# Performance work log

Hardware: AMD Instinct MI355X
Metric: run time of the kernel (lower is better)

Reference implementation:

```python
import jax, jax.numpy as jnp
import numpy as np

N = 100000      # nodes
E = 1600000     # edges (before self-loops)
IN = 128        # in_feats
EF = 64         # edge_feat_size
H = 4           # num_heads
D = 32          # out_feats per head
NEG_SLOPE = 0.2 # DGL GATConv default leaky_relu slope


def setup_inputs() -> dict:
    key = jax.random.key(0)
    ks = jax.random.split(key, 9)
    return {
        "node_feats": jax.random.normal(ks[0], (N, IN), jnp.float32),
        "edge_feats": jax.random.normal(ks[1], (E, EF), jnp.float32),
        "src": jax.random.randint(ks[2], (E,), 0, N),
        "dst": jax.random.randint(ks[3], (E,), 0, N),
        "W_edge": jax.random.normal(ks[4], (EF, IN), jnp.float32) * 0.05,
        "b_edge": jnp.zeros((IN,), jnp.float32),
        "W_fc": jax.random.normal(ks[5], (IN, H * D), jnp.float32) * 0.05,
        "attn_l": jax.random.normal(ks[6], (H, D), jnp.float32) * 0.05,
        "attn_r": jax.random.normal(ks[7], (H, D), jnp.float32) * 0.05,
        "bias": jnp.zeros((H * D,), jnp.float32),
    }


def reference(node_feats, edge_feats, src, dst, W_edge, b_edge, W_fc, attn_l, attn_r, bias):
    # edge_proj: computed in the original forward but NOT consumed by GATConv
    edge_emb = edge_feats @ W_edge + b_edge  # [E, IN] (dead in original module)
    del edge_emb

    # fc projection, split into heads
    feat = (node_feats @ W_fc).reshape(N, H, D)          # [N, H, D]
    el = jnp.einsum('nhd,hd->nh', feat, attn_l)          # [N, H]
    er = jnp.einsum('nhd,hd->nh', feat, attn_r)          # [N, H]

    # add self-loops (dgl.add_self_loop appends (i, i) for every node)
    loops = jnp.arange(N, dtype=src.dtype)
    s = jnp.concatenate([src, loops])                    # [E + N]
    d = jnp.concatenate([dst, loops])                    # [E + N]

    # per-edge attention logits
    e = jax.nn.leaky_relu(el[s] + er[d], NEG_SLOPE)      # [E+N, H]

    # segment softmax over incoming edges of each destination
    emax = jax.ops.segment_max(e, d, num_segments=N)     # [N, H]
    ee = jnp.exp(e - emax[d])                            # [E+N, H]
    denom = jax.ops.segment_sum(ee, d, num_segments=N)   # [N, H]
    alpha = ee / denom[d]                                # [E+N, H]

    # weighted aggregation of source features per destination
    msg = alpha[:, :, None] * feat[s]                    # [E+N, H, D]
    out = jax.ops.segment_sum(msg, d, num_segments=N)    # [N, H, D]
    out = out + bias.reshape(H, D)
    return out
```

## Files before the change

### kernel.cpp

```cpp
#include <hip/hip_runtime.h>
#include <hip/hip_bf16.h>

#define NEG_SLOPE 0.2f

__device__ __forceinline__ int block_scan_incl(int v, int t, int nwaves, int* wsum) {
    const int lane = t & 63, wid = t >> 6;
#pragma unroll
    for (int off = 1; off < 64; off <<= 1) {
        int u = __shfl_up(v, off);
        if (lane >= off) v += u;
    }
    if (lane == 63) wsum[wid] = v;
    __syncthreads();
    if (wid == 0) {
        int w = (lane < nwaves) ? wsum[lane] : 0;
#pragma unroll
        for (int off = 1; off < 64; off <<= 1) {
            int u = __shfl_up(w, off);
            if (lane >= off) w += u;
        }
        if (lane < nwaves) wsum[lane] = w;
    }
    __syncthreads();
    if (wid > 0) v += wsum[wid - 1];
    return v;
}

__global__ __launch_bounds__(256) void gemm_hist_kernel(
    const float* __restrict__ node, const float* __restrict__ Wfc,
    const float* __restrict__ attn_l, const float* __restrict__ attn_r,
    const int* __restrict__ dst, int* __restrict__ counts,
    __hip_bfloat162* __restrict__ featp,
    float* __restrict__ el, float* __restrict__ er,
    int N_, int E_, int T_)
{
    __shared__ float Xl[32][132];
    __shared__ float Wl[32][132];

    const int t  = threadIdx.x;

    for (int e = blockIdx.x * 256 + t; e < T_; e += gridDim.x * 256) {
        int d = (e < E_) ? dst[e] : (e - E_);
        atomicAdd(&counts[d], 1);
    }

    const int tx = t & 15;
    const int ty = t >> 4;
    const int gr0 = blockIdx.x * 128;

    float acc[8][8];
#pragma unroll
    for (int a = 0; a < 8; a++)
#pragma unroll
        for (int b = 0; b < 8; b++) acc[a][b] = 0.f;

    for (int k0 = 0; k0 < 128; k0 += 32) {
#pragma unroll
        for (int j = 0; j < 16; j++) {
            int i = t + 256 * j;
            int kk = i & 31, row = i >> 5;
            int gr = gr0 + row;
            Xl[kk][row] = (gr < N_) ? node[(size_t)gr * 128 + k0 + kk] : 0.f;
        }
#pragma unroll
        for (int j = 0; j < 16; j++) {
            int i = t + 256 * j;
            int kk = i >> 7, c = i & 127;
            Wl[kk][c] = Wfc[(size_t)(k0 + kk) * 128 + c];
        }
        __syncthreads();
#pragma unroll
        for (int kk = 0; kk < 32; kk++) {
            float4 xa = *(const float4*)&Xl[kk][ty * 8];
            float4 xb = *(const float4*)&Xl[kk][ty * 8 + 4];
            float4 wa = *(const float4*)&Wl[kk][tx * 8];
            float4 wb = *(const float4*)&Wl[kk][tx * 8 + 4];
            float xr[8] = {xa.x, xa.y, xa.z, xa.w, xb.x, xb.y, xb.z, xb.w};
            float wc[8] = {wa.x, wa.y, wa.z, wa.w, wb.x, wb.y, wb.z, wb.w};
#pragma unroll
            for (int a = 0; a < 8; a++)
#pragma unroll
                for (int b = 0; b < 8; b++)
                    acc[a][b] = fmaf(xr[a], wc[b], acc[a][b]);
        }
        __syncthreads();
    }

    float al[8], ar[8];
#pragma unroll
    for (int b = 0; b < 8; b++) {
        al[b] = attn_l[tx * 8 + b];
        ar[b] = attn_r[tx * 8 + b];
    }
    const int h = tx >> 2, q = tx & 3;
#pragma unroll
    for (int a = 0; a < 8; a++) {
        int gr = gr0 + ty * 8 + a;
        float pl = 0.f, pr = 0.f;
#pragma unroll
        for (int b = 0; b < 8; b++) {
            pl = fmaf(acc[a][b], al[b], pl);
            pr = fmaf(acc[a][b], ar[b], pr);
        }
        pl += __shfl_xor(pl, 1); pl += __shfl_xor(pl, 2);
        pr += __shfl_xor(pr, 1); pr += __shfl_xor(pr, 2);
        if (gr < N_) {
            union { __hip_bfloat162 h2[4]; float4 f4; } pk;
            pk.h2[0] = __float22bfloat162_rn(make_float2(acc[a][0], acc[a][1]));
            pk.h2[1] = __float22bfloat162_rn(make_float2(acc[a][2], acc[a][3]));
            pk.h2[2] = __float22bfloat162_rn(make_float2(acc[a][4], acc[a][5]));
            pk.h2[3] = __float22bfloat162_rn(make_float2(acc[a][6], acc[a][7]));
            *(float4*)&featp[(size_t)gr * 64 + tx * 4] = pk.f4;
            if (q == 0) { el[gr * 4 + h] = pl; er[gr * 4 + h] = pr; }
        }
    }
}

__global__ __launch_bounds__(1024) void scanA_kernel(
    const int* __restrict__ counts, int* __restrict__ row_start,
    int* __restrict__ partials, int N_)
{
    __shared__ int wsum[16];
    int i = blockIdx.x * 1024 + threadIdx.x;
    int c = (i < N_) ? counts[i] : 0;
    int incl = block_scan_incl(c, threadIdx.x, 16, wsum);
    if (i < N_) row_start[i] = incl - c;
    if (threadIdx.x == 1023) partials[blockIdx.x] = incl;
}

__global__ __launch_bounds__(1024) void scanB_kernel(
    const int* __restrict__ partials, int* __restrict__ offsets,
    int* __restrict__ row_start, int N_, int P)
{
    __shared__ int wsum[16];
    int t = threadIdx.x;
    int v = (t < P) ? partials[t] : 0;
    int incl = block_scan_incl(v, t, 16, wsum);
    if (t < P) offsets[t] = incl - v;
    if (t == 1023) row_start[N_] = incl;
}

__global__ __launch_bounds__(1024) void scanC_kernel(
    int* __restrict__ row_start, int* __restrict__ cursor,
    const int* __restrict__ offsets, int N_)
{
    int i = blockIdx.x * 1024 + threadIdx.x;
    if (i < N_) {
        int v = row_start[i] + offsets[blockIdx.x];
        row_start[i] = v;
        cursor[i] = v;
    }
}

__global__ void scatter_kernel(const int* __restrict__ src, const int* __restrict__ dst,
                               int* __restrict__ cursor, int* __restrict__ sorted_src,
                               int E_, int N_)
{
    int e = blockIdx.x * 256 + threadIdx.x;
    if (e < E_ + N_) {
        int d, s;
        if (e < E_) { d = dst[e]; s = src[e]; }
        else        { d = e - E_; s = e - E_; }
        int pos = atomicAdd(&cursor[d], 1);
        sorted_src[pos] = s;
    }
}

__global__ __launch_bounds__(256) void aggregate_kernel(
    const int* __restrict__ row_start, const int* __restrict__ sorted_src,
    const float* __restrict__ el, const float* __restrict__ er,
    const __hip_bfloat162* __restrict__ featp, const float* __restrict__ bias,
    float* __restrict__ out, int N_)
{
    const int n = blockIdx.x * 4 + (threadIdx.x >> 6);
    if (n >= N_) return;
    const int lane = threadIdx.x & 63;
    const int start = row_start[n];
    const int end   = row_start[n + 1];

    float4 erv = *(const float4*)&er[n * 4];
    float erd[4] = {erv.x, erv.y, erv.z, erv.w};

    float m[4] = {-1e30f, -1e30f, -1e30f, -1e30f};
    float l[4] = {0.f, 0.f, 0.f, 0.f};

    for (int i = start + lane; i < end; i += 64) {
        int s = sorted_src[i];
        float4 ev4 = *(const float4*)&el[(size_t)s * 4];
        float ev[4] = {ev4.x + erd[0], ev4.y + erd[1], ev4.z + erd[2], ev4.w + erd[3]};
#pragma unroll
        for (int hh = 0; hh < 4; hh++) {
            float e = ev[hh] > 0.f ? ev[hh] : NEG_SLOPE * ev[hh];
            if (e > m[hh]) { l[hh] = l[hh] * __expf(m[hh] - e) + 1.f; m[hh] = e; }
            else           { l[hh] += __expf(e - m[hh]); }
        }
    }
    float mloc[4] = {m[0], m[1], m[2], m[3]};
#pragma unroll
    for (int off = 1; off < 64; off <<= 1)
#pragma unroll
        for (int hh = 0; hh < 4; hh++) m[hh] = fmaxf(m[hh], __shfl_xor(m[hh], off));
#pragma unroll
    for (int hh = 0; hh < 4; hh++) l[hh] *= __expf(mloc[hh] - m[hh]);
#pragma unroll
    for (int off = 1; off < 64; off <<= 1)
#pragma unroll
        for (int hh = 0; hh < 4; hh++) l[hh] += __shfl_xor(l[hh], off);

    const int h0 = lane >> 4;
    float M0 = (h0 == 0) ? m[0] : (h0 == 1) ? m[1] : (h0 == 2) ? m[2] : m[3];
    float L0 = (h0 == 0) ? l[0] : (h0 == 1) ? l[1] : (h0 == 2) ? l[2] : l[3];
    float R0 = (h0 == 0) ? erd[0] : (h0 == 1) ? erd[1] : (h0 == 2) ? erd[2] : erd[3];
    const float inv = 1.f / L0;

    float acc0 = 0.f, acc1 = 0.f;
    for (int i = start; i < end; ++i) {
        int s = sorted_src[i];
        float e = el[(size_t)s * 4 + h0] + R0;
        e = e > 0.f ? e : NEG_SLOPE * e;
        float w = __expf(e - M0) * inv;
        float2 f = __bfloat1622float2(featp[(size_t)s * 64 + lane]);
        acc0 = fmaf(w, f.x, acc0);
        acc1 = fmaf(w, f.y, acc1);
    }
    float2 bv = *(const float2*)&bias[2 * lane];
    float2 o = make_float2(acc0 + bv.x, acc1 + bv.y);
    *(float2*)&out[(size_t)n * 128 + 2 * lane] = o;
}

extern "C" void kernel_launch(void* const* d_in, const int* in_sizes, int n_in,
                              void* d_out, int out_size, void* d_ws, size_t ws_size,
                              hipStream_t stream) {
    const float* node   = (const float*)d_in[0];
    const int*   src    = (const int*)d_in[2];
    const int*   dst    = (const int*)d_in[3];
    const float* Wfc    = (const float*)d_in[6];
    const float* attn_l = (const float*)d_in[7];
    const float* attn_r = (const float*)d_in[8];
    const float* bias   = (const float*)d_in[9];
    float* out = (float*)d_out;

    const int N_ = in_sizes[0] / 128;
    const int E_ = in_sizes[2];
    const int T  = E_ + N_;
    const int P  = (N_ + 1023) / 1024;

    auto align256 = [](size_t x) { return (x + 255) & ~(size_t)255; };
    char* ws = (char*)d_ws;
    __hip_bfloat162* featp = (__hip_bfloat162*)ws; ws += align256((size_t)N_ * 64 * 4);
    float* el        = (float*)ws; ws += align256((size_t)N_ * 4 * 4);
    float* er        = (float*)ws; ws += align256((size_t)N_ * 4 * 4);
    int*   counts    = (int*)ws;   ws += align256((size_t)N_ * 4);
    int*   row_start = (int*)ws;   ws += align256((size_t)(N_ + 1) * 4);
    int*   cursor    = (int*)ws;   ws += align256((size_t)N_ * 4);
    int*   partials  = (int*)ws;   ws += align256((size_t)1024 * 4);
    int*   offsets   = (int*)ws;   ws += align256((size_t)1024 * 4);
    int*   sorted    = (int*)ws;   ws += align256((size_t)T * 4);

    hipMemsetAsync(counts, 0, (size_t)N_ * 4, stream);

    gemm_hist_kernel<<<(N_ + 127) / 128, 256, 0, stream>>>(
        node, Wfc, attn_l, attn_r, dst, counts, featp, el, er, N_, E_, T);

    scanA_kernel<<<P, 1024, 0, stream>>>(counts, row_start, partials, N_);
    scanB_kernel<<<1, 1024, 0, stream>>>(partials, offsets, row_start, N_, P);
    scanC_kernel<<<P, 1024, 0, stream>>>(row_start, cursor, offsets, N_);

    scatter_kernel<<<(T + 255) / 256, 256, 0, stream>>>(src, dst, cursor, sorted, E_, N_);

    aggregate_kernel<<<(N_ + 3) / 4, 256, 0, stream>>>(
        row_start, sorted, el, er, featp, bias, out, N_);
}
```

Measured before the change: 1.024 ms.

## Add single-pass LDS fast path for low-degree nodes in GAT aggregation

For destination nodes with at most 64 incoming edges, each lane loads one edge, computes the logits and the exact max and exp weights in one pass, and stores source indices and unnormalized weights in LDS. The aggregation loop then reads from LDS instead of re-reading sorted_src and el from global memory and recomputing the exponentials for every edge. Normalization is moved to a single multiply at the end. High-degree nodes keep the old online-softmax path. The change adds a block-wide barrier and some LDS use per block.

```diff
diff --git a/kernel.cpp b/kernel.cpp
--- a/kernel.cpp
+++ b/kernel.cpp
@@ -172,17 +172,83 @@
     const __hip_bfloat162* __restrict__ featp, const float* __restrict__ bias,
     float* __restrict__ out, int N_)
 {
-    const int n = blockIdx.x * 4 + (threadIdx.x >> 6);
+    __shared__ int   slds[4][64];
+    __shared__ float plds[4][64][4];
+
+    const int wv   = threadIdx.x >> 6;
+    const int lane = threadIdx.x & 63;
+    const int n    = blockIdx.x * 4 + wv;
+
+    int start = 0, deg = 0;
+    float erd[4] = {0.f, 0.f, 0.f, 0.f};
+    if (n < N_) {
+        start = row_start[n];
+        deg   = row_start[n + 1] - start;
+        float4 erv = *(const float4*)&er[(size_t)n * 4];
+        erd[0] = erv.x; erd[1] = erv.y; erd[2] = erv.z; erd[3] = erv.w;
+    }
+
+    const int  h0   = lane >> 4;
+    const bool fast = (n < N_) && (deg <= 64);
+
+    float l[4] = {0.f, 0.f, 0.f, 0.f};
+
+    if (fast) {
+        int s = (lane < deg) ? sorted_src[start + lane] : 0;
+        float4 ev4 = *(const float4*)&el[(size_t)s * 4];
+        float e[4] = {ev4.x + erd[0], ev4.y + erd[1], ev4.z + erd[2], ev4.w + erd[3]};
+#pragma unroll
+        for (int hh = 0; hh < 4; hh++) {
+            float v = e[hh];
+            v = v > 0.f ? v : NEG_SLOPE * v;
+            e[hh] = (lane < deg) ? v : -1e30f;
+        }
+        float m[4] = {e[0], e[1], e[2], e[3]};
+#pragma unroll
+        for (int off = 1; off < 64; off <<= 1)
+#pragma unroll
+            for (int hh = 0; hh < 4; hh++) m[hh] = fmaxf(m[hh], __shfl_xor(m[hh], off));
+        float p[4];
+#pragma unroll
+        for (int hh = 0; hh < 4; hh++) {
+            p[hh] = (lane < deg) ? __expf(e[hh] - m[hh]) : 0.f;
+            l[hh] = p[hh];
+        }
+#pragma unroll
+        for (int off = 1; off < 64; off <<= 1)
+#pragma unroll
+            for (int hh = 0; hh < 4; hh++) l[hh] += __shfl_xor(l[hh], off);
+
+        slds[wv][lane] = s;
+        *(float4*)&plds[wv][lane][0] = make_float4(p[0], p[1], p[2], p[3]);
+    }
+
+    __syncthreads();
+
     if (n >= N_) return;
-    const int lane = threadIdx.x & 63;
-    const int start = row_start[n];
-    const int end   = row_start[n + 1];
-
-    float4 erv = *(const float4*)&er[n * 4];
-    float erd[4] = {erv.x, erv.y, erv.z, erv.w};
+
+    if (fast) {
+        float acc0 = 0.f, acc1 = 0.f;
+#pragma unroll 4
+        for (int i = 0; i < deg; ++i) {
+            int   si = slds[wv][i];
+            float wt = plds[wv][i][h0];
+            float2 f = __bfloat1622float2(featp[(size_t)si * 64 + lane]);
+            acc0 = fmaf(wt, f.x, acc0);
+            acc1 = fmaf(wt, f.y, acc1);
+        }
+        const float L0 = (h0 == 0) ? l[0] : (h0 == 1) ? l[1] : (h0 == 2) ? l[2] : l[3];
+        const float invL = 1.f / L0;
+        float2 bv = *(const float2*)&bias[2 * lane];
+        float2 o = make_float2(fmaf(acc0, invL, bv.x), fmaf(acc1, invL, bv.y));
+        *(float2*)&out[(size_t)n * 128 + 2 * lane] = o;
+        return;
+    }
+
+    const int end = start + deg;
 
     float m[4] = {-1e30f, -1e30f, -1e30f, -1e30f};
-    float l[4] = {0.f, 0.f, 0.f, 0.f};
+    float ll[4] = {0.f, 0.f, 0.f, 0.f};
 
     for (int i = start + lane; i < end; i += 64) {
         int s = sorted_src[i];
@@ -191,8 +257,8 @@
 #pragma unroll
         for (int hh = 0; hh < 4; hh++) {
             float e = ev[hh] > 0.f ? ev[hh] : NEG_SLOPE * ev[hh];
-            if (e > m[hh]) { l[hh] = l[hh] * __expf(m[hh] - e) + 1.f; m[hh] = e; }
-            else           { l[hh] += __expf(e - m[hh]); }
+            if (e > m[hh]) { ll[hh] = ll[hh] * __expf(m[hh] - e) + 1.f; m[hh] = e; }
+            else           { ll[hh] += __expf(e - m[hh]); }
         }
     }
     float mloc[4] = {m[0], m[1], m[2], m[3]};
@@ -201,15 +267,14 @@
 #pragma unroll
         for (int hh = 0; hh < 4; hh++) m[hh] = fmaxf(m[hh], __shfl_xor(m[hh], off));
 #pragma unroll
-    for (int hh = 0; hh < 4; hh++) l[hh] *= __expf(mloc[hh] - m[hh]);
+    for (int hh = 0; hh < 4; hh++) ll[hh] *= __expf(mloc[hh] - m[hh]);
 #pragma unroll
     for (int off = 1; off < 64; off <<= 1)
 #pragma unroll
-        for (int hh = 0; hh < 4; hh++) l[hh] += __shfl_xor(l[hh], off);
-
-    const int h0 = lane >> 4;
+        for (int hh = 0; hh < 4; hh++) ll[hh] += __shfl_xor(ll[hh], off);
+
     float M0 = (h0 == 0) ? m[0] : (h0 == 1) ? m[1] : (h0 == 2) ? m[2] : m[3];
-    float L0 = (h0 == 0) ? l[0] : (h0 == 1) ? l[1] : (h0 == 2) ? l[2] : l[3];
+    float L0 = (h0 == 0) ? ll[0] : (h0 == 1) ? ll[1] : (h0 == 2) ? ll[2] : ll[3];
     float R0 = (h0 == 0) ? erd[0] : (h0 == 1) ? erd[1] : (h0 == 2) ? erd[2] : erd[3];
     const float inv = 1.f / L0;
 
```

Result: faster. 920.2 us (-10.2%).
